# Kernel optimization log

Hardware: AMD Instinct MI355X
Metric: run time of the kernel (lower is better)

Reference implementation:

```python
import jax, jax.numpy as jnp
import numpy as np

NEG_SLOPE = 0.2  # PyG GATConv default negative_slope
EPS = 1e-16      # PyG softmax denominator epsilon


def gat_conv(x, src, dst, W, b, att_src, att_dst, num_nodes):
    """PyG GATConv, heads=1, add_self_loops=True (self loops already in src/dst).
    x: [N, Fin]; src/dst: [E]; W: [Fin, Fout]; att_src/att_dst: [Fout]."""
    h = x @ W                                  # [N, Fout]
    a_src = h @ att_src                        # [N]
    a_dst = h @ att_dst                        # [N]
    e = jax.nn.leaky_relu(a_src[src] + a_dst[dst], NEG_SLOPE)  # [E]
    m = jax.ops.segment_max(e, dst, num_segments=num_nodes)    # softmax over edges grouped by dst
    ex = jnp.exp(e - m[dst])
    denom = jax.ops.segment_sum(ex, dst, num_segments=num_nodes)
    alpha = ex / (denom[dst] + EPS)            # [E]
    out = jax.ops.segment_sum(alpha[:, None] * h[src], dst, num_segments=num_nodes)
    return out + b


def global_attention(x, gate_w, gate_b):
    """PyG GlobalAttention with a single graph: softmax(gate_nn(x)) weighted sum."""
    gate = x @ gate_w + gate_b                 # [N, 1]
    attn = jax.nn.softmax(gate, axis=0)        # softmax over all nodes (one graph)
    return jnp.sum(attn * x, axis=0, keepdims=True)  # [1, F]


def setup_inputs() -> dict:
    key = jax.random.key(0)
    ks = jax.random.split(key, 12)
    N, E, D, H = 50000, 800000, 768, 256
    x = jax.random.normal(ks[0], (N, D), dtype=jnp.float32)
    edge_index = jax.random.randint(ks[1], (2, E), 0, N, dtype=jnp.int64)
    s = 1.0 / np.sqrt(D)
    W1 = jax.random.normal(ks[2], (D, H), dtype=jnp.float32) * s
    b1 = jnp.zeros((H,), dtype=jnp.float32)
    as1 = jax.random.normal(ks[3], (H,), dtype=jnp.float32) * (1.0 / np.sqrt(H))
    ad1 = jax.random.normal(ks[4], (H,), dtype=jnp.float32) * (1.0 / np.sqrt(H))
    s2 = 1.0 / np.sqrt(H)
    W2 = jax.random.normal(ks[5], (H, H), dtype=jnp.float32) * s2
    b2 = jnp.zeros((H,), dtype=jnp.float32)
    as2 = jax.random.normal(ks[6], (H,), dtype=jnp.float32) * s2
    ad2 = jax.random.normal(ks[7], (H,), dtype=jnp.float32) * s2
    gate_w = jax.random.normal(ks[8], (H, 1), dtype=jnp.float32) * s2
    gate_b = jnp.zeros((1,), dtype=jnp.float32)
    return {"x": x, "edge_index": edge_index, "W1": W1, "b1": b1, "as1": as1,
            "ad1": ad1, "W2": W2, "b2": b2, "as2": as2, "ad2": ad2,
            "gate_w": gate_w, "gate_b": gate_b}


def reference(x, edge_index, W1, b1, as1, ad1, W2, b2, as2, ad2, gate_w, gate_b):
    N = x.shape[0]
    loops = jnp.arange(N, dtype=edge_index.dtype)
    src = jnp.concatenate([edge_index[0], loops])  # add self loops (GATConv default)
    dst = jnp.concatenate([edge_index[1], loops])
    h = gat_conv(x, src, dst, W1, b1, as1, ad1, N)
    h = jax.nn.relu(h)
    h = gat_conv(h, src, dst, W2, b2, as2, ad2, N)
    h = jax.nn.relu(h)
    return global_attention(h, gate_w, gate_b)   # [1, 256]
```

## Files before the change

kernel.cpp:

```cpp
#include <hip/hip_runtime.h>

#define WAVE 64
#define LRELU(x) ((x) > 0.0f ? (x) : 0.2f * (x))
#define SB0 __builtin_amdgcn_sched_barrier(0)

typedef __attribute__((ext_vector_type(8))) short bf16x8;
typedef __attribute__((ext_vector_type(8))) unsigned short u16x8;
typedef __attribute__((ext_vector_type(4))) float f32x4;

__device__ __forceinline__ void gld16(const void* g, void* l) {
    __builtin_amdgcn_global_load_lds((const __attribute__((address_space(1))) unsigned int*)g,
                                     (__attribute__((address_space(3))) unsigned int*)l,
                                     16, 0, 0);
}

__device__ __forceinline__ unsigned short f2bf_hi(float f) {
    unsigned u = __builtin_bit_cast(unsigned, f);
    u += 0x7FFF + ((u >> 16) & 1);
    return (unsigned short)(u >> 16);
}

__device__ __forceinline__ bf16x8 rne8(f32x4 a, f32x4 b) {
    bf16x8 h;
    float f[8] = {a[0], a[1], a[2], a[3], b[0], b[1], b[2], b[3]};
#pragma unroll
    for (int e = 0; e < 8; e++) {
        unsigned u = __builtin_bit_cast(unsigned, f[e]);
        u += 0x7FFF + ((u >> 16) & 1);
        h[e] = (short)(u >> 16);
    }
    return h;
}

__global__ __launch_bounds__(512) void k_gemm_f32A(const float* __restrict__ A,
                                                   const unsigned short* __restrict__ Bh,
                                                   unsigned short* __restrict__ Cb,
                                                   float* __restrict__ asrc,
                                                   float* __restrict__ adst,
                                                   const float* __restrict__ att_s,
                                                   const float* __restrict__ att_d,
                                                   int M, int K) {
    __shared__ char smem[73728];

    const int tid = threadIdx.x, lane = tid & 63, w = tid >> 6;
    const int m16 = lane & 15, q = lane >> 4;
    const int mq = w >> 1, nh = w & 1;
    const int row0 = blockIdx.x * 128, col0 = blockIdx.y * 128;
    const int NT = K >> 5;

    f32x4 acc[2][4];
#pragma unroll
    for (int i = 0; i < 2; i++)
#pragma unroll
        for (int j = 0; j < 4; j++) acc[i][j] = (f32x4){0.f, 0.f, 0.f, 0.f};

    const float* apt[2];
    const int jA0 = w * 2;
#pragma unroll
    for (int jj = 0; jj < 2; jj++) {
        int j = jA0 + jj;
        int r = j * 8 + (lane >> 3);
        int grow = row0 + r;
        if (grow > M - 1) grow = M - 1;
        int s = (lane & 7) ^ ((lane >> 3) & 7);
        apt[jj] = A + (size_t)grow * K + s * 4;
    }
    const unsigned short* bpt;
    {
        int r = w * 16 + (lane >> 2);
        int s = (lane & 3) ^ ((lane >> 3) & 3);
        bpt = Bh + (size_t)(col0 + r) * K + s * 8;
    }

    auto stage = [&](int t, int buf) {
        char* S = smem + buf * 24576;
        gld16(bpt + (size_t)t * 32, S + 16384 + w * 1024);
#pragma unroll
        for (int jj = 0; jj < 2; jj++)
            gld16(apt[jj] + (size_t)t * 32, S + (jA0 + jj) * 1024);
    };

    stage(0, 0); SB0;
    stage(1, 1); SB0;
    asm volatile("s_waitcnt vmcnt(3)" ::: "memory");
    __builtin_amdgcn_s_barrier();

    for (int t = 0; t < NT; ++t) {
        if (t + 2 < NT) stage(t + 2, (t + 2) % 3);
        SB0;

        const char* S  = smem + (t % 3) * 24576;
        const char* A_ = S;
        const char* B_ = S + 16384;
        bf16x8 bh[4];
#pragma unroll
        for (int nt = 0; nt < 4; nt++) {
            int r = nh * 64 + nt * 16 + m16;
            int p = q ^ ((r >> 1) & 3);
            bh[nt] = *(const bf16x8*)(B_ + r * 64 + p * 16);
        }
#pragma unroll
        for (int mt = 0; mt < 2; mt++) {
            int r = mq * 32 + mt * 16 + m16;
            int p0 = (2 * q) ^ (r & 7);
            int p1 = (2 * q + 1) ^ (r & 7);
            f32x4 a0 = *(const f32x4*)(A_ + r * 128 + p0 * 16);
            f32x4 a1 = *(const f32x4*)(A_ + r * 128 + p1 * 16);
            bf16x8 ah = rne8(a0, a1);
#pragma unroll
            for (int nt = 0; nt < 4; nt++)
                acc[mt][nt] = __builtin_amdgcn_mfma_f32_16x16x32_bf16(ah, bh[nt], acc[mt][nt], 0, 0, 0);
        }
        SB0;
        if (t + 2 < NT) asm volatile("s_waitcnt vmcnt(3)" ::: "memory");
        else            asm volatile("s_waitcnt vmcnt(0)" ::: "memory");
        __builtin_amdgcn_s_barrier();
    }

    const int rbase = row0 + mq * 32;
    const int cbase = col0 + nh * 64;
#pragma unroll
    for (int mt = 0; mt < 2; mt++)
#pragma unroll
        for (int r = 0; r < 4; r++) {
            int row = rbase + mt * 16 + q * 4 + r;
            if (row < M) {
#pragma unroll
                for (int nt = 0; nt < 4; nt++)
                    Cb[(size_t)row * 256 + cbase + nt * 16 + m16] = f2bf_hi(acc[mt][nt][r]);
            }
        }
    float as_v[4], ad_v[4];
#pragma unroll
    for (int nt = 0; nt < 4; nt++) {
        as_v[nt] = att_s[cbase + nt * 16 + m16];
        ad_v[nt] = att_d[cbase + nt * 16 + m16];
    }
#pragma unroll
    for (int mt = 0; mt < 2; mt++)
#pragma unroll
        for (int r = 0; r < 4; r++) {
            float s = 0.f, d = 0.f;
#pragma unroll
            for (int nt = 0; nt < 4; nt++) {
                float v = acc[mt][nt][r];
                s = fmaf(v, as_v[nt], s);
                d = fmaf(v, ad_v[nt], d);
            }
#pragma unroll
            for (int off = 1; off < 16; off <<= 1) {
                s += __shfl_xor(s, off);
                d += __shfl_xor(d, off);
            }
            int row = rbase + mt * 16 + q * 4 + r;
            if (m16 == 0 && row < M) {
                atomicAdd(&asrc[row], s);
                atomicAdd(&adst[row], d);
            }
        }
}

__global__ __launch_bounds__(512) void k_gemm_bf16A(const unsigned short* __restrict__ Ah,
                                                    const unsigned short* __restrict__ Bh,
                                                    unsigned short* __restrict__ Cb,
                                                    float* __restrict__ asrc,
                                                    float* __restrict__ adst,
                                                    const float* __restrict__ att_s,
                                                    const float* __restrict__ att_d,
                                                    int M, int K) {
    __shared__ char smem[49152];

    const int tid = threadIdx.x, lane = tid & 63, w = tid >> 6;
    const int m16 = lane & 15, q = lane >> 4;
    const int mq = w >> 1, nh = w & 1;
    const int row0 = blockIdx.x * 128, col0 = blockIdx.y * 128;
    const int NT = K >> 5;

    f32x4 acc[2][4];
#pragma unroll
    for (int i = 0; i < 2; i++)
#pragma unroll
        for (int j = 0; j < 4; j++) acc[i][j] = (f32x4){0.f, 0.f, 0.f, 0.f};

    const unsigned short* ahpt;
    const unsigned short* bpt;
    {
        int r = w * 16 + (lane >> 2);
        int s = (lane & 3) ^ ((lane >> 3) & 3);
        ahpt = Ah + (size_t)(row0 + r) * K + s * 8;
        bpt  = Bh + (size_t)(col0 + r) * K + s * 8;
    }

    auto stage = [&](int t, int buf) {
        char* S = smem + buf * 16384;
        gld16(bpt  + (size_t)t * 32, S + 8192 + w * 1024);
        gld16(ahpt + (size_t)t * 32, S + w * 1024);
    };

    stage(0, 0); SB0;
    stage(1, 1); SB0;
    asm volatile("s_waitcnt vmcnt(2)" ::: "memory");
    __builtin_amdgcn_s_barrier();

    for (int t = 0; t < NT; ++t) {
        if (t + 2 < NT) stage(t + 2, (t + 2) % 3);
        SB0;

        const char* S   = smem + (t % 3) * 16384;
        const char* Ah_ = S;
        const char* B_  = S + 8192;
        bf16x8 bh[4];
#pragma unroll
        for (int nt = 0; nt < 4; nt++) {
            int r = nh * 64 + nt * 16 + m16;
            int p = q ^ ((r >> 1) & 3);
            bh[nt] = *(const bf16x8*)(B_ + r * 64 + p * 16);
        }
#pragma unroll
        for (int mt = 0; mt < 2; mt++) {
            int r = mq * 32 + mt * 16 + m16;
            int p = q ^ ((r >> 1) & 3);
            bf16x8 ah = *(const bf16x8*)(Ah_ + r * 64 + p * 16);
#pragma unroll
            for (int nt = 0; nt < 4; nt++)
                acc[mt][nt] = __builtin_amdgcn_mfma_f32_16x16x32_bf16(ah, bh[nt], acc[mt][nt], 0, 0, 0);
        }
        SB0;
        if (t + 2 < NT) asm volatile("s_waitcnt vmcnt(2)" ::: "memory");
        else            asm volatile("s_waitcnt vmcnt(0)" ::: "memory");
        __builtin_amdgcn_s_barrier();
    }

    const int rbase = row0 + mq * 32;
    const int cbase = col0 + nh * 64;
#pragma unroll
    for (int mt = 0; mt < 2; mt++)
#pragma unroll
        for (int r = 0; r < 4; r++) {
            int row = rbase + mt * 16 + q * 4 + r;
            if (row < M) {
#pragma unroll
                for (int nt = 0; nt < 4; nt++)
                    Cb[(size_t)row * 256 + cbase + nt * 16 + m16] = f2bf_hi(acc[mt][nt][r]);
            }
        }
    float as_v[4], ad_v[4];
#pragma unroll
    for (int nt = 0; nt < 4; nt++) {
        as_v[nt] = att_s[cbase + nt * 16 + m16];
        ad_v[nt] = att_d[cbase + nt * 16 + m16];
    }
#pragma unroll
    for (int mt = 0; mt < 2; mt++)
#pragma unroll
        for (int r = 0; r < 4; r++) {
            float s = 0.f, d = 0.f;
#pragma unroll
            for (int nt = 0; nt < 4; nt++) {
                float v = acc[mt][nt][r];
                s = fmaf(v, as_v[nt], s);
                d = fmaf(v, ad_v[nt], d);
            }
#pragma unroll
            for (int off = 1; off < 16; off <<= 1) {
                s += __shfl_xor(s, off);
                d += __shfl_xor(d, off);
            }
            int row = rbase + mt * 16 + q * 4 + r;
            if (m16 == 0 && row < M) {
                atomicAdd(&asrc[row], s);
                atomicAdd(&adst[row], d);
            }
        }
}

__global__ __launch_bounds__(256) void k_convB(const float* __restrict__ W,
                                               unsigned short* __restrict__ BThi, int K) {
    int idx = blockIdx.x * 256 + threadIdx.x;
    int k = idx >> 8, n = idx & 255;
    if (k >= K) return;
    BThi[(size_t)n * K + k] = f2bf_hi(W[(size_t)k * 256 + n]);
}

__global__ __launch_bounds__(256) void k_degree(const int* __restrict__ dst,
                                                int* __restrict__ counts, int E) {
    int e = blockIdx.x * 256 + threadIdx.x;
    if (e < E) atomicAdd(&counts[dst[e]], 1);
}

__global__ __launch_bounds__(256) void k_part(const int* __restrict__ counts,
                                              int* __restrict__ psum, int N) {
    __shared__ int red[256];
    int tid = threadIdx.x;
    int i = blockIdx.x * 256 + tid;
    red[tid] = (i < N) ? counts[i] : 0;
    __syncthreads();
    for (int off = 128; off; off >>= 1) {
        if (tid < off) red[tid] += red[tid + off];
        __syncthreads();
    }
    if (tid == 0) psum[blockIdx.x] = red[0];
}

__global__ __launch_bounds__(256) void k_scan_part(int* __restrict__ psum, int nb,
                                                   int* __restrict__ total_out) {
    __shared__ int s[256];
    int tid = threadIdx.x;
    int v = (tid < nb) ? psum[tid] : 0;
    s[tid] = v;
    __syncthreads();
    for (int off = 1; off < 256; off <<= 1) {
        int t = (tid >= off) ? s[tid - off] : 0;
        __syncthreads();
        s[tid] += t;
        __syncthreads();
    }
    if (tid < nb) psum[tid] = s[tid] - v;
    if (tid == 255) *total_out = s[255];
}

__global__ __launch_bounds__(256) void k_rowptr(const int* __restrict__ counts,
                                                const int* __restrict__ psum,
                                                int* __restrict__ rowptr,
                                                int* __restrict__ cursor, int N) {
    __shared__ int s[256];
    int tid = threadIdx.x;
    int i = blockIdx.x * 256 + tid;
    int v = (i < N) ? counts[i] : 0;
    s[tid] = v;
    __syncthreads();
    for (int off = 1; off < 256; off <<= 1) {
        int t = (tid >= off) ? s[tid - off] : 0;
        __syncthreads();
        s[tid] += t;
        __syncthreads();
    }
    if (i < N) {
        int excl = psum[blockIdx.x] + s[tid] - v;
        rowptr[i] = excl;
        cursor[i] = excl;
    }
}

__global__ __launch_bounds__(256) void k_scatter(const int* __restrict__ src,
                                                 const int* __restrict__ dst,
                                                 int* __restrict__ cursor,
                                                 int* __restrict__ col, int E) {
    int e = blockIdx.x * 256 + threadIdx.x;
    if (e < E) {
        int p = atomicAdd(&cursor[dst[e]], 1);
        col[p] = src[e];
    }
}

__global__ __launch_bounds__(256) void k_edge(const unsigned short* __restrict__ hb,
                                              const float* __restrict__ asrc,
                                              const float* __restrict__ adst,
                                              const float* __restrict__ gmaxv,
                                              const int* __restrict__ rowptr,
                                              const int* __restrict__ col,
                                              const float* __restrict__ bias,
                                              float* __restrict__ outf,
                                              unsigned short* __restrict__ outh,
                                              const float* __restrict__ gw,
                                              const float* __restrict__ gb,
                                              float* __restrict__ gatep, int N) {
    int hw = threadIdx.x >> 5;
    int l  = threadIdx.x & 31;
    int node = blockIdx.x * 8 + hw;
    if (node >= N) return;
    int j = rowptr[node], end = rowptr[node + 1];
    float ad = adst[node];
    float m = LRELU(gmaxv[0] + ad);

    float a[8];
    float wself = __expf(LRELU(asrc[node] + ad) - m);
    u16x8 hv = *(const u16x8*)&hb[(size_t)node * 256 + l * 8];
#pragma unroll
    for (int e = 0; e < 8; e++)
        a[e] = wself * __builtin_bit_cast(float, (unsigned)hv[e] << 16);
    float denom = wself;

    for (; j + 4 <= end; j += 4) {
        int s0 = col[j], s1 = col[j + 1], s2 = col[j + 2], s3 = col[j + 3];
        float w0 = __expf(LRELU(asrc[s0] + ad) - m);
        float w1 = __expf(LRELU(asrc[s1] + ad) - m);
        float w2 = __expf(LRELU(asrc[s2] + ad) - m);
        float w3 = __expf(LRELU(asrc[s3] + ad) - m);
        denom += w0 + w1 + w2 + w3;
        u16x8 h0 = *(const u16x8*)&hb[(size_t)s0 * 256 + l * 8];
        u16x8 h1 = *(const u16x8*)&hb[(size_t)s1 * 256 + l * 8];
        u16x8 h2 = *(const u16x8*)&hb[(size_t)s2 * 256 + l * 8];
        u16x8 h3 = *(const u16x8*)&hb[(size_t)s3 * 256 + l * 8];
#pragma unroll
        for (int e = 0; e < 8; e++) {
            float f0 = __builtin_bit_cast(float, (unsigned)h0[e] << 16);
            float f1 = __builtin_bit_cast(float, (unsigned)h1[e] << 16);
            float f2 = __builtin_bit_cast(float, (unsigned)h2[e] << 16);
            float f3 = __builtin_bit_cast(float, (unsigned)h3[e] << 16);
            a[e] = fmaf(w0, f0, fmaf(w1, f1, fmaf(w2, f2, fmaf(w3, f3, a[e]))));
        }
    }
    for (; j < end; j++) {
        int s = col[j];
        float wgt = __expf(LRELU(asrc[s] + ad) - m);
        denom += wgt;
        u16x8 hx = *(const u16x8*)&hb[(size_t)s * 256 + l * 8];
#pragma unroll
        for (int e = 0; e < 8; e++)
            a[e] = fmaf(wgt, __builtin_bit_cast(float, (unsigned)hx[e] << 16), a[e]);
    }
    float inv = 1.0f / (denom + 1e-16f);
#pragma unroll
    for (int e = 0; e < 8; e++) a[e] *= inv;

    float o[8];
    {
        float4 bv0 = *(const float4*)&bias[l * 8];
        float4 bv1 = *(const float4*)&bias[l * 8 + 4];
        float bb[8] = {bv0.x, bv0.y, bv0.z, bv0.w, bv1.x, bv1.y, bv1.z, bv1.w};
#pragma unroll
        for (int e = 0; e < 8; e++) o[e] = fmaxf(a[e] + bb[e], 0.0f);
    }
    if (outf) {
        float4 o0 = make_float4(o[0], o[1], o[2], o[3]);
        float4 o1 = make_float4(o[4], o[5], o[6], o[7]);
        *(float4*)&outf[(size_t)node * 256 + l * 8]     = o0;
        *(float4*)&outf[(size_t)node * 256 + l * 8 + 4] = o1;
    }
    if (outh) {
        u16x8 ph;
#pragma unroll
        for (int e = 0; e < 8; e++) ph[e] = f2bf_hi(o[e]);
        *(u16x8*)&outh[(size_t)node * 256 + l * 8] = ph;
    }
    if (gatep) {
        float s = 0.f;
#pragma unroll
        for (int e = 0; e < 8; e++) s = fmaf(o[e], gw[l * 8 + e], s);
#pragma unroll
        for (int off = 16; off; off >>= 1) s += __shfl_xor(s, off);
        if (l == 0) gatep[node] = s + gb[0];
    }
}

__global__ __launch_bounds__(256) void k_pmax(const float* __restrict__ v, int N,
                                              float* __restrict__ pmax) {
    __shared__ float red[256];
    int tid = threadIdx.x;
    float m = -3.0e38f;
    for (int i = blockIdx.x * 256 + tid; i < N; i += gridDim.x * 256) m = fmaxf(m, v[i]);
    red[tid] = m;
    __syncthreads();
    for (int off = 128; off; off >>= 1) {
        if (tid < off) red[tid] = fmaxf(red[tid], red[tid + off]);
        __syncthreads();
    }
    if (tid == 0) pmax[blockIdx.x] = red[0];
}

__global__ __launch_bounds__(64) void k_fold(const float* __restrict__ p,
                                             float* __restrict__ o) {
    int lane = threadIdx.x;
    float m = p[lane];
#pragma unroll
    for (int off = 32; off; off >>= 1) m = fmaxf(m, __shfl_xor(m, off));
    if (lane == 0) o[0] = m;
}

__global__ __launch_bounds__(256) void k_gmid(const float* __restrict__ pmax, int nb,
                                              float* __restrict__ scal,
                                              float* __restrict__ gout) {
    __shared__ float red[256];
    int tid = threadIdx.x;
    red[tid] = (tid < nb) ? pmax[tid] : -3.0e38f;
    __syncthreads();
    for (int off = 128; off; off >>= 1) {
        if (tid < off) red[tid] = fmaxf(red[tid], red[tid + off]);
        __syncthreads();
    }
    if (tid == 0) { scal[0] = red[0]; scal[1] = 0.0f; }
    gout[tid] = 0.0f;
}

__global__ __launch_bounds__(256) void k_gout(const float* __restrict__ h,
                                              const float* __restrict__ gate,
                                              float* __restrict__ scal_rw,
                                              float* __restrict__ gout, int N) {
    int f = threadIdx.x;
    float gmax = scal_rw[0];
    float acc = 0.0f, sumw = 0.0f;
    for (int i = blockIdx.x; i < N; i += gridDim.x) {
        float w = __expf(gate[i] - gmax);
        acc = fmaf(w, h[(size_t)i * 256 + f], acc);
        sumw += w;
    }
    atomicAdd(&gout[f], acc);
    if (f == 0) atomicAdd(&scal_rw[1], sumw);
}

__global__ __launch_bounds__(256) void k_final(const float* __restrict__ gout,
                                               const float* __restrict__ scal,
                                               float* __restrict__ out) {
    int f = threadIdx.x;
    out[f] = gout[f] / scal[1];
}

extern "C" void kernel_launch(void* const* d_in, const int* in_sizes, int n_in,
                              void* d_out, int out_size, void* d_ws, size_t ws_size,
                              hipStream_t stream) {
    const float* x   = (const float*)d_in[0];
    const int*   ei  = (const int*)d_in[1];
    const float* W1  = (const float*)d_in[2];
    const float* b1  = (const float*)d_in[3];
    const float* as1 = (const float*)d_in[4];
    const float* ad1 = (const float*)d_in[5];
    const float* W2  = (const float*)d_in[6];
    const float* b2  = (const float*)d_in[7];
    const float* as2 = (const float*)d_in[8];
    const float* ad2 = (const float*)d_in[9];
    const float* gw  = (const float*)d_in[10];
    const float* gb  = (const float*)d_in[11];
    float* out = (float*)d_out;

    const int N = in_sizes[0] / 768;
    const int E = in_sizes[1] / 2;
    const int Mpad = (N + 127) & ~127;
    const int* srcA = ei;
    const int* dstA = ei + E;

    char* w = (char*)d_ws;
    auto alloc = [&](size_t bytes) -> void* {
        void* p = (void*)w;
        w += (bytes + 255) & ~(size_t)255;
        return p;
    };
    unsigned short* bufHb = (unsigned short*)alloc((size_t)N * 256 * 2);
    float* bufX = (float*)alloc((size_t)Mpad * 256 * 4);
    unsigned short* X2h = (unsigned short*)bufX;
    float* asrc   = (float*)alloc((size_t)N * 4);
    float* adst   = (float*)alloc((size_t)N * 4);
    float* gate   = (float*)alloc((size_t)N * 4);
    int*   counts = (int*)alloc((size_t)N * 4);
    int*   rowptr = (int*)alloc((size_t)(N + 1) * 4);
    int*   cursor = (int*)alloc((size_t)N * 4);
    int*   colbuf = (int*)alloc((size_t)E * 4);
    int*   psum   = (int*)alloc(256 * 4);
    float* pmax   = (float*)alloc(256 * 4);
    float* gmaxv  = (float*)alloc(4 * 4);
    float* scal   = (float*)alloc(8 * 4);
    float* gout   = (float*)alloc(256 * 4);
    unsigned short* BT1 = (unsigned short*)alloc((size_t)256 * 768 * 2);
    unsigned short* BT2 = (unsigned short*)alloc((size_t)256 * 256 * 2);

    const int eb  = (E + 255) / 256;
    const int nb8 = (N + 7) / 8;
    const int nb  = (N + 255) / 256;
    const dim3 gg(Mpad / 128, 2);

    k_convB<<<768, 256, 0, stream>>>(W1, BT1, 768);
    k_convB<<<256, 256, 0, stream>>>(W2, BT2, 256);

    (void)hipMemsetAsync(counts, 0, (size_t)N * 4, stream);
    k_degree<<<eb, 256, 0, stream>>>(dstA, counts, E);
    k_part<<<nb, 256, 0, stream>>>(counts, psum, N);
    k_scan_part<<<1, 256, 0, stream>>>(psum, nb, rowptr + N);
    k_rowptr<<<nb, 256, 0, stream>>>(counts, psum, rowptr, cursor, N);
    k_scatter<<<eb, 256, 0, stream>>>(srcA, dstA, cursor, colbuf, E);

    (void)hipMemsetAsync(asrc, 0, (size_t)N * 4, stream);
    (void)hipMemsetAsync(adst, 0, (size_t)N * 4, stream);
    k_gemm_f32A<<<gg, 512, 0, stream>>>(x, BT1, bufHb, asrc, adst, as1, ad1, N, 768);
    k_pmax<<<64, 256, 0, stream>>>(asrc, N, pmax);
    k_fold<<<1, 64, 0, stream>>>(pmax, gmaxv);
    k_edge<<<nb8, 256, 0, stream>>>(bufHb, asrc, adst, gmaxv, rowptr, colbuf, b1,
                                    nullptr, X2h, nullptr, nullptr, nullptr, N);

    (void)hipMemsetAsync(asrc, 0, (size_t)N * 4, stream);
    (void)hipMemsetAsync(adst, 0, (size_t)N * 4, stream);
    k_gemm_bf16A<<<gg, 512, 0, stream>>>(X2h, BT2, bufHb, asrc, adst, as2, ad2, N, 256);
    k_pmax<<<64, 256, 0, stream>>>(asrc, N, pmax);
    k_fold<<<1, 64, 0, stream>>>(pmax, gmaxv);
    k_edge<<<nb8, 256, 0, stream>>>(bufHb, asrc, adst, gmaxv, rowptr, colbuf, b2,
                                    bufX, nullptr, gw, gb, gate, N);

    k_pmax<<<64, 256, 0, stream>>>(gate, N, pmax);
    k_gmid<<<1, 256, 0, stream>>>(pmax, 64, scal, gout);
    k_gout<<<256, 256, 0, stream>>>(bufX, gate, scal, gout, N);
    k_final<<<1, 256, 0, stream>>>(gout, scal, out);
}
```

Before: 588.1 us.

## Give each wave private LDS staging buffers and drop per-iteration block barriers

The f32-A GEMM now lets each wave stage its own 32-row A slice and 64-row B slice into a private LDS region, double-buffered, instead of sharing a triple-buffered block tile. Because no wave reads another wave's data, the per-iteration s_barrier is removed and waves synchronise only with their own vmcnt waits. Next-tile loads are issued after the LDS reads complete, so they overlap with the MFMAs. The cost is redundant global loads, since waves sharing rows or columns each fetch them, and LDS use grows to 128KB, which limits occupancy to one block per CU.

```diff
diff --git a/kernel.cpp b/kernel.cpp
--- a/kernel.cpp
+++ b/kernel.cpp
@@ -40,7 +40,7 @@
                                                    const float* __restrict__ att_s,
                                                    const float* __restrict__ att_d,
                                                    int M, int K) {
-    __shared__ char smem[73728];
+    __shared__ char smem[131072];
 
     const int tid = threadIdx.x, lane = tid & 63, w = tid >> 6;
     const int m16 = lane & 15, q = lane >> 4;
@@ -48,73 +48,82 @@
     const int row0 = blockIdx.x * 128, col0 = blockIdx.y * 128;
     const int NT = K >> 5;
 
+    char* Wp   = smem + w * 16384;
+    char* Abuf = Wp;
+    char* Bbuf = Wp + 8192;
+
     f32x4 acc[2][4];
 #pragma unroll
     for (int i = 0; i < 2; i++)
 #pragma unroll
         for (int j = 0; j < 4; j++) acc[i][j] = (f32x4){0.f, 0.f, 0.f, 0.f};
 
-    const float* apt[2];
-    const int jA0 = w * 2;
-#pragma unroll
-    for (int jj = 0; jj < 2; jj++) {
-        int j = jA0 + jj;
-        int r = j * 8 + (lane >> 3);
-        int grow = row0 + r;
+    const float* apt[4];
+#pragma unroll
+    for (int j = 0; j < 4; j++) {
+        int rl = j * 8 + (lane >> 3);
+        int grow = row0 + mq * 32 + rl;
         if (grow > M - 1) grow = M - 1;
         int s = (lane & 7) ^ ((lane >> 3) & 7);
-        apt[jj] = A + (size_t)grow * K + s * 4;
-    }
-    const unsigned short* bpt;
-    {
-        int r = w * 16 + (lane >> 2);
+        apt[j] = A + (size_t)grow * K + s * 4;
+    }
+    const unsigned short* bpt[4];
+#pragma unroll
+    for (int j = 0; j < 4; j++) {
+        int bl = j * 16 + (lane >> 2);
         int s = (lane & 3) ^ ((lane >> 3) & 3);
-        bpt = Bh + (size_t)(col0 + r) * K + s * 8;
-    }
-
-    auto stage = [&](int t, int buf) {
-        char* S = smem + buf * 24576;
-        gld16(bpt + (size_t)t * 32, S + 16384 + w * 1024);
-#pragma unroll
-        for (int jj = 0; jj < 2; jj++)
-            gld16(apt[jj] + (size_t)t * 32, S + (jA0 + jj) * 1024);
+        bpt[j] = Bh + (size_t)(col0 + nh * 64 + bl) * K + s * 8;
+    }
+
+    auto stageA = [&](int t) {
+        char* D = Abuf + (t & 1) * 4096;
+#pragma unroll
+        for (int j = 0; j < 4; j++) gld16(apt[j] + (size_t)t * 32, D + j * 1024);
     };
-
-    stage(0, 0); SB0;
-    stage(1, 1); SB0;
-    asm volatile("s_waitcnt vmcnt(3)" ::: "memory");
-    __builtin_amdgcn_s_barrier();
+    auto stageB = [&](int t) {
+        char* D = Bbuf + (t & 1) * 4096;
+#pragma unroll
+        for (int j = 0; j < 4; j++) gld16(bpt[j] + (size_t)t * 32, D + j * 1024);
+    };
+
+    stageB(0); SB0;
+    stageA(0); SB0;
+    stageA(1); SB0;
 
     for (int t = 0; t < NT; ++t) {
-        if (t + 2 < NT) stage(t + 2, (t + 2) % 3);
+        if (t + 1 < NT) asm volatile("s_waitcnt vmcnt(4)" ::: "memory");
+        else            asm volatile("s_waitcnt vmcnt(0)" ::: "memory");
         SB0;
-
-        const char* S  = smem + (t % 3) * 24576;
-        const char* A_ = S;
-        const char* B_ = S + 16384;
+        const char* A_ = Abuf + (t & 1) * 4096;
+        const char* B_ = Bbuf + (t & 1) * 4096;
         bf16x8 bh[4];
 #pragma unroll
         for (int nt = 0; nt < 4; nt++) {
-            int r = nh * 64 + nt * 16 + m16;
-            int p = q ^ ((r >> 1) & 3);
-            bh[nt] = *(const bf16x8*)(B_ + r * 64 + p * 16);
-        }
+            int bl = nt * 16 + m16;
+            int p = q ^ ((bl >> 1) & 3);
+            bh[nt] = *(const bf16x8*)(B_ + bl * 64 + p * 16);
+        }
+        f32x4 a0[2], a1[2];
 #pragma unroll
         for (int mt = 0; mt < 2; mt++) {
-            int r = mq * 32 + mt * 16 + m16;
-            int p0 = (2 * q) ^ (r & 7);
-            int p1 = (2 * q + 1) ^ (r & 7);
-            f32x4 a0 = *(const f32x4*)(A_ + r * 128 + p0 * 16);
-            f32x4 a1 = *(const f32x4*)(A_ + r * 128 + p1 * 16);
-            bf16x8 ah = rne8(a0, a1);
+            int rl = mt * 16 + m16;
+            int p0 = (2 * q) ^ (rl & 7);
+            int p1 = (2 * q + 1) ^ (rl & 7);
+            a0[mt] = *(const f32x4*)(A_ + rl * 128 + p0 * 16);
+            a1[mt] = *(const f32x4*)(A_ + rl * 128 + p1 * 16);
+        }
+        asm volatile("s_waitcnt lgkmcnt(0)" ::: "memory");
+        SB0;
+        if (t + 1 < NT) stageB(t + 1);
+        if (t + 2 < NT) stageA(t + 2);
+        SB0;
+#pragma unroll
+        for (int mt = 0; mt < 2; mt++) {
+            bf16x8 ah = rne8(a0[mt], a1[mt]);
 #pragma unroll
             for (int nt = 0; nt < 4; nt++)
                 acc[mt][nt] = __builtin_amdgcn_mfma_f32_16x16x32_bf16(ah, bh[nt], acc[mt][nt], 0, 0, 0);
         }
-        SB0;
-        if (t + 2 < NT) asm volatile("s_waitcnt vmcnt(3)" ::: "memory");
-        else            asm volatile("s_waitcnt vmcnt(0)" ::: "memory");
-        __builtin_amdgcn_s_barrier();
     }
 
     const int rbase = row0 + mq * 32;
```

After: 629.2 us. 7.0% more time.
